# Kernel tuning notes

Measured on AMD Instinct MI355X. Metric: run time of the kernel, lower is better.

The kernel has to match this reference:

```python
import jax, jax.numpy as jnp
import numpy as np

B, NIN, M = 4, 4096, 16384
CIN, COUT = 256, 128
EPS_BN = 1e-5


def _mlp(x, w, b, g, beta, rm, rv):
    # x: (B, Cin, N); w: (Cout, Cin) -- Conv1d kernel_size=1
    y = jnp.einsum('oi,bin->bon', w, x) + b[:, None]
    y = g[:, None] * (y - rm[:, None]) / jnp.sqrt(rv[:, None] + EPS_BN) + beta[:, None]
    return jax.nn.relu(y)


def setup_inputs() -> dict:
    key = jax.random.key(0)
    ks = jax.random.split(key, 12)
    inp = {
        'rgb': jax.random.normal(ks[0], (B, CIN, NIN), jnp.float32),
        'xyzin': jax.random.normal(ks[1], (B, NIN, 3), jnp.float32),
        'xyzout': jax.random.normal(ks[2], (B, M, 3), jnp.float32),
        'w1': jax.random.normal(ks[3], (COUT, CIN), jnp.float32) * (1.0 / np.sqrt(CIN)),
        'b1': jnp.zeros((COUT,), jnp.float32),
        'g1': jnp.ones((COUT,), jnp.float32),
        'beta1': jnp.zeros((COUT,), jnp.float32),
        'rm1': jnp.zeros((COUT,), jnp.float32),
        'rv1': jnp.ones((COUT,), jnp.float32),
        'w2': jax.random.normal(ks[4], (COUT, COUT), jnp.float32) * (1.0 / np.sqrt(COUT)),
        'b2': jnp.zeros((COUT,), jnp.float32),
        'g2': jnp.ones((COUT,), jnp.float32),
        'beta2': jnp.zeros((COUT,), jnp.float32),
        'rm2': jnp.zeros((COUT,), jnp.float32),
        'rv2': jnp.ones((COUT,), jnp.float32),
        'w3': jax.random.normal(ks[5], (COUT, COUT), jnp.float32) * (1.0 / np.sqrt(COUT)),
        'b3': jnp.zeros((COUT,), jnp.float32),
        'g3': jnp.zeros((COUT,), jnp.float32) + 1.0,
        'beta3': jnp.zeros((COUT,), jnp.float32),
        'rm3': jnp.zeros((COUT,), jnp.float32),
        'rv3': jnp.ones((COUT,), jnp.float32),
    }
    return inp


def reference(rgb, xyzin, xyzout,
              w1, b1, g1, beta1, rm1, rv1,
              w2, b2, g2, beta2, rm2, rv2,
              w3, b3, g3, beta3, rm3, rv3):
    # 3 pointwise MLP blocks (Conv1d k=1 + BN + ReLU)
    feat = _mlp(rgb, w1, b1, g1, beta1, rm1, rv1)
    feat = _mlp(feat, w2, b2, g2, beta2, rm2, rv2)
    feat = _mlp(feat, w3, b3, g3, beta3, rm3, rv3)  # (B, COUT, NIN)

    # squared pairwise distances (B, M, NIN), clamped like the torch code:
    # get_dists clamps <0 to 1e-7 then sqrt; forward then squares -> clamped d^2
    d2 = (jnp.sum(xyzout * xyzout, -1)[:, :, None]
          + jnp.sum(xyzin * xyzin, -1)[:, None, :]
          - 2.0 * jnp.einsum('bmc,bnc->bmn', xyzout, xyzin))
    d2 = jnp.where(d2 < 0, jnp.float32(1e-7), d2)

    # top-3 smallest distances (== first 3 of full ascending sort)
    neg_vals, idx = jax.lax.top_k(-d2, 3)  # (B, M, 3)
    wv = 1.0 / (-neg_vals)
    wv = wv / jnp.sum(wv, -1, keepdims=True)

    # gather neighbor features: feat^T is (B, NIN, COUT)
    featT = jnp.transpose(feat, (0, 2, 1))
    nb = jnp.take_along_axis(featT, idx.reshape(B, M * 3, 1), axis=1)
    nb = nb.reshape(B, M, 3, COUT)

    out = jnp.einsum('bmk,bmkc->bmc', wv, nb)  # weighted interpolation
    return jnp.transpose(out, (0, 2, 1))  # (B, COUT, M)
```

## Files before the change

kernel.cpp:

```cpp
#include <hip/hip_runtime.h>
#include <hip/hip_bf16.h>
#include <cstdint>
#include <cstddef>

constexpr int BB   = 4;
constexpr int NIN  = 4096;
constexpr int MM   = 16384;
constexpr int CIN  = 256;
constexpr int COUT = 128;
constexpr float EPSBN = 1e-5f;

__global__ __launch_bounds__(256) void prep_kernel(
    const float* __restrict__ w1, const float* __restrict__ w2, const float* __restrict__ w3,
    const float* __restrict__ b1, const float* __restrict__ g1, const float* __restrict__ be1,
    const float* __restrict__ rm1, const float* __restrict__ rv1,
    const float* __restrict__ b2, const float* __restrict__ g2, const float* __restrict__ be2,
    const float* __restrict__ rm2, const float* __restrict__ rv2,
    const float* __restrict__ b3, const float* __restrict__ g3, const float* __restrict__ be3,
    const float* __restrict__ rm3, const float* __restrict__ rv3,
    const float* __restrict__ xyzin,
    float* __restrict__ WT1, float* __restrict__ WT2, float* __restrict__ WT3,
    float* __restrict__ st, float4* __restrict__ packed)
{
    int tid  = blockIdx.x * blockDim.x + threadIdx.x;
    int nthr = gridDim.x * blockDim.x;

    for (int i = tid; i < CIN * COUT; i += nthr)
        WT1[i] = w1[(i & 127) * CIN + (i >> 7)];
    for (int i = tid; i < COUT * COUT; i += nthr)
        WT2[i] = w2[(i & 127) * COUT + (i >> 7)];
    for (int i = tid; i < COUT * COUT; i += nthr)
        WT3[i] = w3[(i & 127) * COUT + (i >> 7)];

    for (int i = tid; i < 3 * COUT; i += nthr) {
        int l = i >> 7, o = i & 127;
        const float* bb = (l == 0) ? b1 : (l == 1) ? b2 : b3;
        const float* gg = (l == 0) ? g1 : (l == 1) ? g2 : g3;
        const float* be = (l == 0) ? be1 : (l == 1) ? be2 : be3;
        const float* rm = (l == 0) ? rm1 : (l == 1) ? rm2 : rm3;
        const float* rv = (l == 0) ? rv1 : (l == 1) ? rv2 : rv3;
        float s = gg[o] / sqrtf(rv[o] + EPSBN);
        st[l * 256 + o]       = s;
        st[l * 256 + 128 + o] = s * (bb[o] - rm[o]) + be[o];
    }

    for (int i = tid; i < BB * NIN; i += nthr) {
        float x = xyzin[i * 3 + 0], y = xyzin[i * 3 + 1], z = xyzin[i * 3 + 2];
        float sn = __fadd_rn(__fadd_rn(__fmul_rn(x, x), __fmul_rn(y, y)), __fmul_rn(z, z));
        packed[i] = make_float4(2.0f * x, 2.0f * y, 2.0f * z, sn);
    }
}

template <int CI, bool TOUT>
__global__ __launch_bounds__(256) void mlp_kernel(
    const float* __restrict__ in, const float* __restrict__ WT,
    const float* __restrict__ svec, const float* __restrict__ tvec,
    float* __restrict__ out)
{
    __shared__ float Xs[32][32];
    __shared__ float Ws[32][128];

    int blk = blockIdx.x;
    int b   = blk >> 7;
    int n0  = (blk & 127) * 32;
    int t   = threadIdx.x;
    int og  = t & 31;
    int ng  = t >> 5;

    float acc[4][4] = {};
    const float* inb = in + (size_t)b * CI * NIN;

    for (int k0 = 0; k0 < CI; k0 += 32) {
        __syncthreads();
        {
            int r = t >> 3, c = (t & 7) * 4;
            *(float4*)&Xs[r][c] = *(const float4*)&inb[(size_t)(k0 + r) * NIN + n0 + c];
        }
        #pragma unroll
        for (int r = 0; r < 4; ++r) {
            int e = (r * 256 + t) * 4;
            *(float4*)&Ws[0][e] = *(const float4*)&WT[(size_t)k0 * 128 + e];
        }
        __syncthreads();
        #pragma unroll
        for (int kk = 0; kk < 32; ++kk) {
            float w[4], xv[4];
            *(float4*)w  = *(const float4*)&Ws[kk][og * 4];
            *(float4*)xv = *(const float4*)&Xs[kk][ng * 4];
            #pragma unroll
            for (int oi = 0; oi < 4; ++oi)
                #pragma unroll
                for (int j = 0; j < 4; ++j)
                    acc[oi][j] = fmaf(w[oi], xv[j], acc[oi][j]);
        }
    }

    #pragma unroll
    for (int oi = 0; oi < 4; ++oi) {
        float s  = svec[og * 4 + oi];
        float tt = tvec[og * 4 + oi];
        #pragma unroll
        for (int j = 0; j < 4; ++j)
            acc[oi][j] = fmaxf(fmaf(s, acc[oi][j], tt), 0.0f);
    }

    if (TOUT) {
        #pragma unroll
        for (int j = 0; j < 4; ++j) {
            int n = n0 + ng * 4 + j;
            float4 v = make_float4(acc[0][j], acc[1][j], acc[2][j], acc[3][j]);
            *(float4*)&out[((size_t)(b * NIN + n)) * COUT + og * 4] = v;
        }
    } else {
        #pragma unroll
        for (int oi = 0; oi < 4; ++oi) {
            int o = og * 4 + oi;
            float4 v = make_float4(acc[oi][0], acc[oi][1], acc[oi][2], acc[oi][3]);
            *(float4*)&out[((size_t)b * COUT + o) * NIN + n0 + ng * 4] = v;
        }
    }
}

__global__ __launch_bounds__(512) void knn_kernel(
    const float4* __restrict__ packed, const float* __restrict__ xyzout,
    float* __restrict__ topw, int* __restrict__ topi)
{
    __shared__ float PD[8][64][3];
    __shared__ int   PI[8][64][3];

    int b  = blockIdx.y;
    int m0 = blockIdx.x * 64;
    int t  = threadIdx.x;
    int ml = t & 63, q = t >> 6;
    int m  = m0 + ml;

    size_t ob = ((size_t)b * MM + m) * 3;
    float x = xyzout[ob], y = xyzout[ob + 1], z = xyzout[ob + 2];
    float sm = __fadd_rn(__fadd_rn(__fmul_rn(x, x), __fmul_rn(y, y)), __fmul_rn(z, z));

    int qs = __builtin_amdgcn_readfirstlane(q);
    int nbase = qs * 512;
    const float4* pb = packed + (size_t)b * NIN + nbase;

    float e0 = 3.402823466e38f, e1 = 3.402823466e38f, e2 = 3.402823466e38f;
    int j0 = 0, j1 = 0, j2 = 0;

    for (int i0 = 0; i0 < 512; i0 += 8) {
        float4 pv[8];
        #pragma unroll
        for (int u = 0; u < 8; ++u) pv[u] = pb[i0 + u];
        #pragma unroll
        for (int u = 0; u < 8; ++u) {
            float4 p = pv[u];
            float dot2 = __fadd_rn(__fadd_rn(__fmul_rn(x, p.x), __fmul_rn(y, p.y)), __fmul_rn(z, p.z));
            float d    = __fsub_rn(__fadd_rn(sm, p.w), dot2);
            if (d < e2) {
                int n = nbase + i0 + u;
                bool lt0 = d < e0, lt1 = d < e1;
                j2 = lt1 ? j1 : n;
                j1 = lt1 ? (lt0 ? j0 : n) : j1;
                j0 = lt0 ? n : j0;
                e2 = __builtin_amdgcn_fmed3f(d, e1, e2);
                e1 = __builtin_amdgcn_fmed3f(d, e0, e1);
                e0 = fminf(e0, d);
            }
        }
    }

    PD[q][ml][0] = e0; PD[q][ml][1] = e1; PD[q][ml][2] = e2;
    PI[q][ml][0] = j0; PI[q][ml][1] = j1; PI[q][ml][2] = j2;
    __syncthreads();

    if (t < 64) {
        float f0 = 3.402823466e38f, f1 = 3.402823466e38f, f2 = 3.402823466e38f;
        int i0 = 0, i1 = 0, i2 = 0;
        #pragma unroll
        for (int qq = 0; qq < 8; ++qq) {
            #pragma unroll
            for (int k = 0; k < 3; ++k) {
                float d = PD[qq][t][k];
                int   n = PI[qq][t][k];
                bool lt0 = d < f0, lt1 = d < f1, lt2 = d < f2;
                i2 = lt2 ? (lt1 ? i1 : n) : i2;
                i1 = lt1 ? (lt0 ? i0 : n) : i1;
                i0 = lt0 ? n : i0;
                f2 = __builtin_amdgcn_fmed3f(d, f1, f2);
                f1 = __builtin_amdgcn_fmed3f(d, f0, f1);
                f0 = fminf(f0, d);
            }
        }
        f0 = fmaxf(f0, 1e-7f); f1 = fmaxf(f1, 1e-7f); f2 = fmaxf(f2, 1e-7f);
        float iv0 = 1.0f / f0, iv1 = 1.0f / f1, iv2 = 1.0f / f2;
        float s = iv0 + iv1 + iv2;
        size_t wb = ((size_t)b * MM + m0 + t) * 3;
        topw[wb + 0] = iv0 / s; topw[wb + 1] = iv1 / s; topw[wb + 2] = iv2 / s;
        topi[wb + 0] = i0;      topi[wb + 1] = i1;      topi[wb + 2] = i2;
    }
}

__global__ __launch_bounds__(256) void interp_kernel(
    const float* __restrict__ featT, const float* __restrict__ topw,
    const int* __restrict__ topi, float* __restrict__ out)
{
    __shared__ float G[32][388];
    __shared__ float Wl[32][4];

    int b  = blockIdx.y;
    int m0 = blockIdx.x * 32;
    int t  = threadIdx.x;

    if (t < 96) {
        int mm = t / 3, k = t - (t / 3) * 3;
        Wl[mm][k] = topw[((size_t)b * MM + m0 + mm) * 3 + k];
    }
    int lane = t & 31, r8 = t >> 5;
    #pragma unroll
    for (int pass = 0; pass < 12; ++pass) {
        int r  = pass * 8 + r8;
        int mm = r / 3, k = r - (r / 3) * 3;
        int idx = topi[((size_t)b * MM + m0 + mm) * 3 + k];
        const float4 v = *(const float4*)&featT[((size_t)(b * NIN + idx)) * COUT + lane * 4];
        *(float4*)&G[mm][k * 128 + lane * 4] = v;
    }
    __syncthreads();

    int m  = t & 31;
    int obq = (t >> 5) * 16;
    float w0 = Wl[m][0], w1 = Wl[m][1], w2 = Wl[m][2];
    const float* Gm = &G[m][0];
    size_t outbase = ((size_t)b * COUT) * MM + m0 + m;
    #pragma unroll
    for (int oi = 0; oi < 16; ++oi) {
        int o = obq + oi;
        float v = w0 * Gm[o] + w1 * Gm[128 + o] + w2 * Gm[256 + o];
        out[outbase + (size_t)o * MM] = v;
    }
}

extern "C" void kernel_launch(void* const* d_in, const int* in_sizes, int n_in,
                              void* d_out, int out_size, void* d_ws, size_t ws_size,
                              hipStream_t stream)
{
    const float* rgb    = (const float*)d_in[0];
    const float* xyzin  = (const float*)d_in[1];
    const float* xyzout = (const float*)d_in[2];
    const float* w1  = (const float*)d_in[3];
    const float* b1  = (const float*)d_in[4];
    const float* g1  = (const float*)d_in[5];
    const float* be1 = (const float*)d_in[6];
    const float* rm1 = (const float*)d_in[7];
    const float* rv1 = (const float*)d_in[8];
    const float* w2  = (const float*)d_in[9];
    const float* b2  = (const float*)d_in[10];
    const float* g2  = (const float*)d_in[11];
    const float* be2 = (const float*)d_in[12];
    const float* rm2 = (const float*)d_in[13];
    const float* rv2 = (const float*)d_in[14];
    const float* w3  = (const float*)d_in[15];
    const float* b3  = (const float*)d_in[16];
    const float* g3  = (const float*)d_in[17];
    const float* be3 = (const float*)d_in[18];
    const float* rm3 = (const float*)d_in[19];
    const float* rv3 = (const float*)d_in[20];
    float* out = (float*)d_out;

    float* ws   = (float*)d_ws;
    float* WT1  = ws;
    float* WT2  = WT1 + 32768;
    float* WT3  = WT2 + 16384;
    float* st   = WT3 + 16384;
    float4* packed = (float4*)(st + 768);
    float* featA = st + 768 + 65536;
    float* featB = featA + 2097152;
    float* topw  = featB + 2097152;
    int*   topi  = (int*)(topw + 196608);

    prep_kernel<<<256, 256, 0, stream>>>(w1, w2, w3,
        b1, g1, be1, rm1, rv1,
        b2, g2, be2, rm2, rv2,
        b3, g3, be3, rm3, rv3,
        xyzin, WT1, WT2, WT3, st, packed);

    mlp_kernel<CIN, false><<<dim3(BB * (NIN / 32)), 256, 0, stream>>>(
        rgb, WT1, st + 0, st + 128, featA);
    mlp_kernel<COUT, false><<<dim3(BB * (NIN / 32)), 256, 0, stream>>>(
        featA, WT2, st + 256, st + 384, featB);
    mlp_kernel<COUT, true><<<dim3(BB * (NIN / 32)), 256, 0, stream>>>(
        featB, WT3, st + 512, st + 640, featA);

    knn_kernel<<<dim3(MM / 64, BB), 512, 0, stream>>>(packed, xyzout, topw, topi);

    interp_kernel<<<dim3(MM / 32, BB), 256, 0, stream>>>(featA, topw, topi, out);
}
```

Measured before the change: 251.3 us.

## Double-buffer MLP tiles with async global-to-LDS loads

The MLP GEMM kernel now uses two LDS buffers and issues the next K-tile's input and weight loads with direct global-to-LDS loads (global_load_lds, 16 bytes) before computing on the current tile. One barrier per iteration replaces the two used before. The goal is to overlap memory latency with the FMA loop and to skip the register staging of the copy. This doubles LDS use, and correctness depends on the async loads finishing before the barrier and on the wave-contiguous LDS address layout.

```diff
diff --git a/kernel.cpp b/kernel.cpp
--- a/kernel.cpp
+++ b/kernel.cpp
@@ -9,6 +9,12 @@
 constexpr int CIN  = 256;
 constexpr int COUT = 128;
 constexpr float EPSBN = 1e-5f;
+
+typedef __attribute__((address_space(1))) const uint32_t gu32;
+typedef __attribute__((address_space(3))) uint32_t lu32;
+__device__ __forceinline__ void gload16(const float* g, float* l) {
+    __builtin_amdgcn_global_load_lds((gu32*)g, (lu32*)l, 16, 0, 0);
+}
 
 __global__ __launch_bounds__(256) void prep_kernel(
     const float* __restrict__ w1, const float* __restrict__ w2, const float* __restrict__ w3,
@@ -57,8 +63,8 @@
     const float* __restrict__ svec, const float* __restrict__ tvec,
     float* __restrict__ out)
 {
-    __shared__ float Xs[32][32];
-    __shared__ float Ws[32][128];
+    __shared__ float Xs[2][32][32];
+    __shared__ float Ws[2][32][128];
 
     int blk = blockIdx.x;
     int b   = blk >> 7;
@@ -67,32 +73,49 @@
     int og  = t & 31;
     int ng  = t >> 5;
 
+    const float* inb = in + (size_t)b * CI * NIN;
+
+    int xr = t >> 3, xc = (t & 7) * 4;
+    const float* gx_base = &inb[(size_t)xr * NIN + n0 + xc];
+    float* lx0 = &Xs[0][xr][xc];
+    float* lx1 = &Xs[1][xr][xc];
+
     float acc[4][4] = {};
-    const float* inb = in + (size_t)b * CI * NIN;
-
+
+    gload16(gx_base, lx0);
+    #pragma unroll
+    for (int r = 0; r < 4; ++r) {
+        int e = (r * 256 + t) * 4;
+        gload16(WT + e, &Ws[0][0][0] + e);
+    }
+    __syncthreads();
+
+    int buf = 0;
     for (int k0 = 0; k0 < CI; k0 += 32) {
-        __syncthreads();
-        {
-            int r = t >> 3, c = (t & 7) * 4;
-            *(float4*)&Xs[r][c] = *(const float4*)&inb[(size_t)(k0 + r) * NIN + n0 + c];
-        }
-        #pragma unroll
-        for (int r = 0; r < 4; ++r) {
-            int e = (r * 256 + t) * 4;
-            *(float4*)&Ws[0][e] = *(const float4*)&WT[(size_t)k0 * 128 + e];
-        }
-        __syncthreads();
+        if (k0 + 32 < CI) {
+            if (buf == 0) gload16(gx_base + (size_t)(k0 + 32) * NIN, lx1);
+            else          gload16(gx_base + (size_t)(k0 + 32) * NIN, lx0);
+            const float* gw = WT + (size_t)(k0 + 32) * 128;
+            float* lw = &Ws[buf ^ 1][0][0];
+            #pragma unroll
+            for (int r = 0; r < 4; ++r) {
+                int e = (r * 256 + t) * 4;
+                gload16(gw + e, lw + e);
+            }
+        }
         #pragma unroll
         for (int kk = 0; kk < 32; ++kk) {
             float w[4], xv[4];
-            *(float4*)w  = *(const float4*)&Ws[kk][og * 4];
-            *(float4*)xv = *(const float4*)&Xs[kk][ng * 4];
+            *(float4*)w  = *(const float4*)&Ws[buf][kk][og * 4];
+            *(float4*)xv = *(const float4*)&Xs[buf][kk][ng * 4];
             #pragma unroll
             for (int oi = 0; oi < 4; ++oi)
                 #pragma unroll
                 for (int j = 0; j < 4; ++j)
                     acc[oi][j] = fmaf(w[oi], xv[j], acc[oi][j]);
         }
+        __syncthreads();
+        buf ^= 1;
     }
 
     #pragma unroll
```

After: 256.9 us. 2.2% more time.
